# Kernel optimization log

Measured on AMD Instinct MI355X. Metric: run time of the kernel, lower is better.

The kernel has to match this reference:

```python
import jax, jax.numpy as jnp
import numpy as np

K = 8192
D = 512


def setup_inputs() -> dict:
    key = jax.random.key(0)
    k1, k2 = jax.random.split(key)
    x = jax.random.normal(k1, (32, 512, D), dtype=jnp.float32)
    # nn.Embedding weight init: uniform(-1/k, 1/k)
    codebook = jax.random.uniform(k2, (K, D), dtype=jnp.float32,
                                  minval=-1.0 / K, maxval=1.0 / K)
    return {"x": x, "codebook": codebook}


def reference(x, codebook):
    # flatten to [N, D]
    z_e = x.reshape(-1, x.shape[-1])
    # squared L2 distances: ||z||^2 - 2 z c^T + ||c||^2  -> [N, K]
    dists = (jnp.sum(z_e * z_e, axis=1, keepdims=True)
             - 2.0 * jnp.einsum('nd,kd->nk', z_e, codebook)
             + jnp.sum(codebook * codebook, axis=1)[None, :])
    indices = jnp.argmin(dists, axis=1)  # [N]
    z_q = codebook[indices]              # [N, D] gather
    # straight-through estimator: forward z_q, grad passes to z_e
    z_q_st = z_e + jax.lax.stop_gradient(z_q - z_e)
    # vq loss pulls codebook toward (detached) encoder outputs
    vq_loss = jnp.mean((z_q - jax.lax.stop_gradient(z_e)) ** 2)
    # commitment loss pulls encoder outputs toward (detached) codes
    commit_loss = jnp.mean((z_e - jax.lax.stop_gradient(z_q)) ** 2)
    z_q_out = z_q_st.reshape(x.shape)
    idx_out = indices.reshape(x.shape[:-1])
    return z_q_out, vq_loss, commit_loss, idx_out
```

## Files before the change

kernel.cpp:

```cpp
#include <hip/hip_runtime.h>

#define K_CODES 8192
#define D_DIM   512
#define N_ROWS  16384
#define NSPLIT  32
#define CAP     8
#define T2      2.0e-4f
#define LIST_CAP 32768

typedef __attribute__((ext_vector_type(8))) short bf16x8;
typedef __attribute__((ext_vector_type(4))) float f32x4;
typedef unsigned char uchar;
typedef unsigned short ushort;
typedef unsigned long long u64;

__device__ __forceinline__ unsigned fkey(float f) {
    unsigned b = __float_as_uint(f);
    return (b & 0x80000000u) ? ~b : (b | 0x80000000u);
}
__device__ __forceinline__ float finv(unsigned k) {
    return __uint_as_float((k & 0x80000000u) ? (k & 0x7fffffffu) : ~k);
}

__device__ __forceinline__ unsigned pk_bf16(float a, float b) {
    unsigned ua = __float_as_uint(a), ub = __float_as_uint(b);
    ua = (ua + 0x7fffu + ((ua >> 16) & 1u)) >> 16;
    ub = (ub + 0x7fffu + ((ub >> 16) & 1u)) & 0xffff0000u;
    return ua | ub;
}

__device__ __forceinline__ void gload_lds16(const void* g, void* l) {
    __builtin_amdgcn_global_load_lds(
        (const __attribute__((address_space(1))) unsigned int*)g,
        (__attribute__((address_space(3))) unsigned int*)l, 16, 0, 0);
}

__global__ void vq_prepass(const float* __restrict__ x, const float* __restrict__ cb,
                           unsigned* __restrict__ xb, unsigned* __restrict__ cbb,
                           float* __restrict__ sn, u64* __restrict__ keys,
                           int* __restrict__ count) {
    const int bid = blockIdx.x;
    const int t = threadIdx.x;
    if (bid < 6144) {
        const size_t gid = (size_t)bid * 256 + t;
        const size_t nx = (size_t)N_ROWS * D_DIM / 8;
        if (gid < nx) {
            const float4 f0 = ((const float4*)x)[gid * 2];
            const float4 f1 = ((const float4*)x)[gid * 2 + 1];
            ((uint4*)xb)[gid] = make_uint4(pk_bf16(f0.x, f0.y), pk_bf16(f0.z, f0.w),
                                           pk_bf16(f1.x, f1.y), pk_bf16(f1.z, f1.w));
        } else {
            const size_t g = gid - nx;
            const float4 f0 = ((const float4*)cb)[g * 2];
            const float4 f1 = ((const float4*)cb)[g * 2 + 1];
            ((uint4*)cbb)[g] = make_uint4(pk_bf16(f0.x, f0.y), pk_bf16(f0.z, f0.w),
                                          pk_bf16(f1.x, f1.y), pk_bf16(f1.z, f1.w));
        }
    } else {
        const int base = (bid - 6144) * 8;
        if (bid == 6144 && t == 0) *count = 0;
        if (t < 8) keys[base + t] = ~0ull;
        const int wave = t >> 6, lane = t & 63;
        const int row = base + wave * 2 + (lane >> 5);
        const int l = lane & 31, b = l >> 3, j = l & 7;
        const float* a = x + (size_t)row * D_DIM + b * 128 + j;
        float r = __fmul_rn(a[0], a[0]);
#pragma unroll
        for (int i = 1; i < 16; ++i) {
            const float v = a[i * 8];
            r = __fadd_rn(r, __fmul_rn(v, v));
        }
        r = __fadd_rn(r, __shfl_xor(r, 1));
        r = __fadd_rn(r, __shfl_xor(r, 2));
        r = __fadd_rn(r, __shfl_xor(r, 4));
        r = __fadd_rn(r, __shfl_xor(r, 8));
        r = __fadd_rn(r, __shfl_xor(r, 16));
        if (l == 0) sn[row] = r;
    }
}

__global__ __launch_bounds__(256)
void vq_sn(const float* __restrict__ x, float* __restrict__ sn,
           u64* __restrict__ keys, int* __restrict__ count) {
    const int t = threadIdx.x;
    const int base = blockIdx.x * 8;
    if (blockIdx.x == 0 && t == 0) *count = 0;
    if (t < 8) keys[base + t] = ~0ull;
    const int wave = t >> 6, lane = t & 63;
    const int row = base + wave * 2 + (lane >> 5);
    const int l = lane & 31, b = l >> 3, j = l & 7;
    const float* a = x + (size_t)row * D_DIM + b * 128 + j;
    float r = __fmul_rn(a[0], a[0]);
#pragma unroll
    for (int i = 1; i < 16; ++i) {
        const float v = a[i * 8];
        r = __fadd_rn(r, __fmul_rn(v, v));
    }
    r = __fadd_rn(r, __shfl_xor(r, 1));
    r = __fadd_rn(r, __shfl_xor(r, 2));
    r = __fadd_rn(r, __shfl_xor(r, 4));
    r = __fadd_rn(r, __shfl_xor(r, 8));
    r = __fadd_rn(r, __shfl_xor(r, 16));
    if (l == 0) sn[row] = r;
}

template<bool PRE>
__global__ __launch_bounds__(256, 2)
void vq_screen2(const float* __restrict__ x, const float* __restrict__ cb,
                const ushort* __restrict__ xb, const ushort* __restrict__ cbb,
                float* __restrict__ g_dmax, uchar* __restrict__ g_cnt,
                uchar* __restrict__ g_cand) {
    __shared__ ushort Ash[2][128 * 32];
    __shared__ ushort Bsh[2][256 * 32];
    __shared__ unsigned vkey[128];
    __shared__ int ccnt[128];
    __shared__ uchar clist[128][CAP];

    const int t    = threadIdx.x;
    const int w    = t >> 6, lane = t & 63;
    const int fr   = lane & 15;
    const int quad = lane >> 4;
    const int wr   = (w & 1) * 64;
    const int wc   = (w >> 1) * 128;
    const int row0  = blockIdx.y * 128;
    const int kbase = blockIdx.x * 256;

    if (t < 128) { vkey[t] = 0u; ccnt[t] = 0; }

    int aoff[4], boff[8];
#pragma unroll
    for (int i = 0; i < 4; ++i) {
        const int rw = wr + i * 16 + fr;
        aoff[i] = rw * 32 + ((quad ^ (rw >> 1)) & 3) * 8;
    }
#pragma unroll
    for (int j = 0; j < 8; ++j) {
        const int rw = wc + j * 16 + fr;
        boff[j] = rw * 32 + ((quad ^ (rw >> 1)) & 3) * 8;
    }

    f32x4 acc[4][8];
#pragma unroll
    for (int i = 0; i < 4; ++i)
#pragma unroll
        for (int j = 0; j < 8; ++j) acc[i][j] = (f32x4)0.0f;

    if (PRE) {
        const int la = lane >> 2;
        const int p  = lane & 3;
        const int ia0 = w * 2 + 0, rA0 = ia0 * 16 + la;
        const int ia1 = w * 2 + 1, rA1 = ia1 * 16 + la;
        const char* srcA0 = (const char*)xb + (size_t)(row0 + rA0) * 1024 + ((p ^ ((rA0 >> 1) & 3)) * 16);
        const char* srcA1 = (const char*)xb + (size_t)(row0 + rA1) * 1024 + ((p ^ ((rA1 >> 1) & 3)) * 16);
        const int dA0 = ia0 * 512, dA1 = ia1 * 512;
        const int ib0 = w * 4 + 0, rB0 = ib0 * 16 + la;
        const int ib1 = w * 4 + 1, rB1 = ib1 * 16 + la;
        const int ib2 = w * 4 + 2, rB2 = ib2 * 16 + la;
        const int ib3 = w * 4 + 3, rB3 = ib3 * 16 + la;
        const char* srcB0 = (const char*)cbb + (size_t)(kbase + rB0) * 1024 + ((p ^ ((rB0 >> 1) & 3)) * 16);
        const char* srcB1 = (const char*)cbb + (size_t)(kbase + rB1) * 1024 + ((p ^ ((rB1 >> 1) & 3)) * 16);
        const char* srcB2 = (const char*)cbb + (size_t)(kbase + rB2) * 1024 + ((p ^ ((rB2 >> 1) & 3)) * 16);
        const char* srcB3 = (const char*)cbb + (size_t)(kbase + rB3) * 1024 + ((p ^ ((rB3 >> 1) & 3)) * 16);

#define STAGE6(buf, slab) do {                                     \
        gload_lds16(srcA0 + (slab) * 64, &Ash[buf][dA0]);          \
        gload_lds16(srcA1 + (slab) * 64, &Ash[buf][dA1]);          \
        gload_lds16(srcB0 + (slab) * 64, &Bsh[buf][dB0]);          \
        gload_lds16(srcB1 + (slab) * 64, &Bsh[buf][dB1]);          \
        gload_lds16(srcB2 + (slab) * 64, &Bsh[buf][dB2]);          \
        gload_lds16(srcB3 + (slab) * 64, &Bsh[buf][dB3]);          \
    } while (0)
        const int dB0 = ib0 * 512, dB1 = ib1 * 512, dB2 = ib2 * 512, dB3 = ib3 * 512;

        STAGE6(0, 0);
        asm volatile("s_waitcnt vmcnt(0)" ::: "memory");
        __builtin_amdgcn_s_barrier();

#pragma unroll 2
        for (int dc = 0; dc < 16; ++dc) {
            const int cur = dc & 1;
            if (dc < 15) STAGE6(cur ^ 1, dc + 1);
            bf16x8 af[4], bfv[8];
#pragma unroll
            for (int i = 0; i < 4; ++i) af[i] = *(const bf16x8*)&Ash[cur][aoff[i]];
#pragma unroll
            for (int j = 0; j < 8; ++j) bfv[j] = *(const bf16x8*)&Bsh[cur][boff[j]];
#pragma unroll
            for (int i = 0; i < 4; ++i)
#pragma unroll
                for (int j = 0; j < 8; ++j)
                    acc[i][j] = __builtin_amdgcn_mfma_f32_16x16x32_bf16(af[i], bfv[j], acc[i][j], 0, 0, 0);
            asm volatile("s_waitcnt vmcnt(0)" ::: "memory");
            __builtin_amdgcn_s_barrier();
        }
#undef STAGE6
    } else {
        const int r = t >> 1, h = t & 1;
        const int sA = (r >> 1) & 3;
        const int ca0 = (2 * h) ^ sA;
        ushort* awp0 = &Ash[0][r * 32 + ca0 * 8];
        ushort* awp1 = &Ash[0][r * 32 + (ca0 ^ 1) * 8];
        const int sB = (t >> 1) & 3;
        ushort* bwp0 = &Bsh[0][t * 32 + (0 ^ sB) * 8];
        ushort* bwp1 = &Bsh[0][t * 32 + (1 ^ sB) * 8];
        ushort* bwp2 = &Bsh[0][t * 32 + (2 ^ sB) * 8];
        ushort* bwp3 = &Bsh[0][t * 32 + (3 ^ sB) * 8];
        const char* gA = (const char*)(x  + (size_t)(row0 + r) * D_DIM + h * 16);
        const char* gB = (const char*)(cb + (size_t)(kbase + t) * D_DIM);
        for (int dc = 0; dc < 16; ++dc) {
            const float4* fa = (const float4*)(gA + dc * 128);
            float4 f0 = fa[0], f1 = fa[1], f2 = fa[2], f3 = fa[3];
            uint4 a0 = make_uint4(pk_bf16(f0.x, f0.y), pk_bf16(f0.z, f0.w),
                                  pk_bf16(f1.x, f1.y), pk_bf16(f1.z, f1.w));
            uint4 a1 = make_uint4(pk_bf16(f2.x, f2.y), pk_bf16(f2.z, f2.w),
                                  pk_bf16(f3.x, f3.y), pk_bf16(f3.z, f3.w));
            const float4* fb = (const float4*)(gB + dc * 128);
            float4 g0 = fb[0], g1 = fb[1], g2 = fb[2], g3 = fb[3];
            float4 g4 = fb[4], g5 = fb[5], g6 = fb[6], g7 = fb[7];
            uint4 b0 = make_uint4(pk_bf16(g0.x, g0.y), pk_bf16(g0.z, g0.w),
                                  pk_bf16(g1.x, g1.y), pk_bf16(g1.z, g1.w));
            uint4 b1 = make_uint4(pk_bf16(g2.x, g2.y), pk_bf16(g2.z, g2.w),
                                  pk_bf16(g3.x, g3.y), pk_bf16(g3.z, g3.w));
            uint4 b2 = make_uint4(pk_bf16(g4.x, g4.y), pk_bf16(g4.z, g4.w),
                                  pk_bf16(g5.x, g5.y), pk_bf16(g5.z, g5.w));
            uint4 b3 = make_uint4(pk_bf16(g6.x, g6.y), pk_bf16(g6.z, g6.w),
                                  pk_bf16(g7.x, g7.y), pk_bf16(g7.z, g7.w));
            __syncthreads();
            *(uint4*)awp0 = a0; *(uint4*)awp1 = a1;
            *(uint4*)bwp0 = b0; *(uint4*)bwp1 = b1;
            *(uint4*)bwp2 = b2; *(uint4*)bwp3 = b3;
            __syncthreads();
            bf16x8 af[4], bfv[8];
#pragma unroll
            for (int i = 0; i < 4; ++i) af[i] = *(const bf16x8*)&Ash[0][aoff[i]];
#pragma unroll
            for (int j = 0; j < 8; ++j) bfv[j] = *(const bf16x8*)&Bsh[0][boff[j]];
#pragma unroll
            for (int i = 0; i < 4; ++i)
#pragma unroll
                for (int j = 0; j < 8; ++j)
                    acc[i][j] = __builtin_amdgcn_mfma_f32_16x16x32_bf16(af[i], bfv[j], acc[i][j], 0, 0, 0);
        }
    }

    __syncthreads();
#pragma unroll
    for (int i = 0; i < 4; ++i)
#pragma unroll
        for (int rg = 0; rg < 4; ++rg) {
            float m = acc[i][0][rg];
#pragma unroll
            for (int j = 1; j < 8; ++j) m = fmaxf(m, acc[i][j][rg]);
            m = fmaxf(m, __shfl_xor(m, 1));
            m = fmaxf(m, __shfl_xor(m, 2));
            m = fmaxf(m, __shfl_xor(m, 4));
            m = fmaxf(m, __shfl_xor(m, 8));
            if (fr == 0) atomicMax(&vkey[wr + i * 16 + quad * 4 + rg], fkey(m));
        }
    __syncthreads();
#pragma unroll
    for (int i = 0; i < 4; ++i)
#pragma unroll
        for (int rg = 0; rg < 4; ++rg) {
            const int row = wr + i * 16 + quad * 4 + rg;
            const float thr = finv(vkey[row]) - T2;
#pragma unroll
            for (int j = 0; j < 8; ++j) {
                if (acc[i][j][rg] >= thr) {
                    int p = atomicAdd(&ccnt[row], 1);
                    if (p < CAP) clist[row][p] = (uchar)(wc + j * 16 + fr);
                }
            }
        }
    __syncthreads();
    if (t < 128) {
        const size_t o = (size_t)(row0 + t) * NSPLIT + blockIdx.x;
        g_dmax[o] = finv(vkey[t]);
        int c = ccnt[t];
        g_cnt[o] = (uchar)(c > 255 ? 255 : c);
        ((uint2*)g_cand)[o] = *(const uint2*)clist[t];
    }
}

__global__ __launch_bounds__(256)
void vq_build(const float* __restrict__ g_dmax, const uchar* __restrict__ g_cnt,
              const uchar* __restrict__ g_cand, int2* __restrict__ list,
              int* __restrict__ count, float* __restrict__ idx_f) {
    const int row = blockIdx.x * blockDim.x + threadIdx.x;
    const int lane = threadIdx.x & 63;
    const float* dm = g_dmax + (size_t)row * NSPLIT;
    float g = dm[0];
#pragma unroll
    for (int s = 1; s < NSPLIT; ++s) g = fmaxf(g, dm[s]);
    const float thr = g - T2;

    int tot = 0, first = -1;
    for (int s = 0; s < NSPLIT; ++s) {
        if (dm[s] < thr) continue;
        const size_t o = (size_t)row * NSPLIT + s;
        const int c = g_cnt[o];
        tot += (c > CAP) ? 256 : c;
        if (first < 0) first = s * 256 + g_cand[o * CAP];
    }
    idx_f[row] = (float)first;

    const int need = (tot > 1) ? tot : 0;
    int scan = need;
#pragma unroll
    for (int d = 1; d < 64; d <<= 1) {
        const int v = __shfl_up(scan, d, 64);
        if (lane >= d) scan += v;
    }
    const int wtot = __shfl(scan, 63, 64);
    int base = 0;
    if (lane == 63 && wtot > 0) base = atomicAdd(count, wtot);
    base = __shfl(base, 63, 64);
    if (need == 0) return;
    int pos = base + scan - need;

    for (int s = 0; s < NSPLIT; ++s) {
        if (dm[s] < thr) continue;
        const size_t o = (size_t)row * NSPLIT + s;
        const int c = g_cnt[o];
        if (c > CAP) {
            for (int u = 0; u < 256; ++u, ++pos)
                if (pos < LIST_CAP) list[pos] = make_int2(row, s * 256 + u);
        } else {
            for (int u = 0; u < c; ++u, ++pos)
                if (pos < LIST_CAP) list[pos] = make_int2(row, s * 256 + g_cand[o * CAP + u]);
        }
    }
}

__device__ __forceinline__ float np_einsum_dot(const float* __restrict__ a,
                                               const float* __restrict__ b) {
    float S0 = 0.f, S1 = 0.f, S2 = 0.f, S3 = 0.f;
    for (int i = 0; i < D_DIM; i += 16) {
        S0 = __fadd_rn(S0, __fmul_rn(a[i + 12], b[i + 12]));
        S1 = __fadd_rn(S1, __fmul_rn(a[i + 13], b[i + 13]));
        S2 = __fadd_rn(S2, __fmul_rn(a[i + 14], b[i + 14]));
        S3 = __fadd_rn(S3, __fmul_rn(a[i + 15], b[i + 15]));
        S0 = __fadd_rn(S0, __fmul_rn(a[i +  8], b[i +  8]));
        S1 = __fadd_rn(S1, __fmul_rn(a[i +  9], b[i +  9]));
        S2 = __fadd_rn(S2, __fmul_rn(a[i + 10], b[i + 10]));
        S3 = __fadd_rn(S3, __fmul_rn(a[i + 11], b[i + 11]));
        S0 = __fadd_rn(S0, __fmul_rn(a[i +  4], b[i +  4]));
        S1 = __fadd_rn(S1, __fmul_rn(a[i +  5], b[i +  5]));
        S2 = __fadd_rn(S2, __fmul_rn(a[i +  6], b[i +  6]));
        S3 = __fadd_rn(S3, __fmul_rn(a[i +  7], b[i +  7]));
        S0 = __fadd_rn(S0, __fmul_rn(a[i +  0], b[i +  0]));
        S1 = __fadd_rn(S1, __fmul_rn(a[i +  1], b[i +  1]));
        S2 = __fadd_rn(S2, __fmul_rn(a[i +  2], b[i +  2]));
        S3 = __fadd_rn(S3, __fmul_rn(a[i +  3], b[i +  3]));
    }
    return __fadd_rn(__fadd_rn(S0, S1), __fadd_rn(S2, S3));
}

__global__ __launch_bounds__(256)
void vq_replay(const float* __restrict__ x, const float* __restrict__ cb,
               const float* __restrict__ sn, const int2* __restrict__ list,
               const int* __restrict__ count, u64* __restrict__ keys) {
    const int i = blockIdx.x * blockDim.x + threadIdx.x;
    int n = *count; if (n > LIST_CAP) n = LIST_CAP;
    if (i >= n) return;
    const int2 e = list[i];
    const float* zr = x + (size_t)e.x * D_DIM;
    const float d = __fadd_rn(sn[e.x],
                              __fmul_rn(-2.0f, np_einsum_dot(zr, cb + (size_t)e.y * D_DIM)));
    const u64 key = ((u64)fkey(d) << 32) | (unsigned)e.y;
    atomicMin(&keys[e.x], key);
}

__global__ void vq_gather_kernel(const float* __restrict__ x,
                                 const float* __restrict__ cb,
                                 const u64* __restrict__ keys,
                                 float* __restrict__ idx_f,
                                 float* __restrict__ zq_out,
                                 double* __restrict__ psum) {
    const int row = blockIdx.x;
    const int t   = threadIdx.x;
    const u64 ky = keys[row];
    const int k = (ky != ~0ull) ? (int)(ky & 0xffffffffu) : (int)idx_f[row];
    const float4 c  = ((const float4*)(cb + (size_t)k   * D_DIM))[t];
    const float4 xv = ((const float4*)(x  + (size_t)row * D_DIM))[t];
    float4 o;
    o.x = __fadd_rn(xv.x, __fsub_rn(c.x, xv.x));
    o.y = __fadd_rn(xv.y, __fsub_rn(c.y, xv.y));
    o.z = __fadd_rn(xv.z, __fsub_rn(c.z, xv.z));
    o.w = __fadd_rn(xv.w, __fsub_rn(c.w, xv.w));
    ((float4*)(zq_out + (size_t)row * D_DIM))[t] = o;
    const double d0 = (double)c.x - (double)xv.x;
    const double d1 = (double)c.y - (double)xv.y;
    const double d2 = (double)c.z - (double)xv.z;
    const double d3 = (double)c.w - (double)xv.w;
    double s = d0 * d0 + d1 * d1 + d2 * d2 + d3 * d3;
#pragma unroll
    for (int off = 32; off > 0; off >>= 1) s += __shfl_xor(s, off, 64);
    __shared__ double red[2];
    if ((t & 63) == 0) red[t >> 6] = s;
    __syncthreads();
    if (t == 0) {
        psum[row] = red[0] + red[1];
        idx_f[row] = (float)k;
    }
}

__global__ void vq_finalize2(const double* __restrict__ psum,
                             float* __restrict__ losses) {
    __shared__ double red[4];
    const int t = threadIdx.x;
    double s = 0.0;
    for (int i = t; i < N_ROWS; i += 256) s += psum[i];
#pragma unroll
    for (int off = 32; off > 0; off >>= 1) s += __shfl_xor(s, off, 64);
    if ((t & 63) == 0) red[t >> 6] = s;
    __syncthreads();
    if (t == 0) {
        const double tot = red[0] + red[1] + red[2] + red[3];
        const float l = (float)(tot / (double)((size_t)N_ROWS * D_DIM));
        losses[0] = l;
        losses[1] = l;
    }
}

extern "C" void kernel_launch(void* const* d_in, const int* in_sizes, int n_in,
                              void* d_out, int out_size, void* d_ws, size_t ws_size,
                              hipStream_t stream) {
    const float* x  = (const float*)d_in[0];
    const float* cb = (const float*)d_in[1];
    float* out    = (float*)d_out;
    float* zq     = out;
    float* losses = out + (size_t)N_ROWS * D_DIM;
    float* idx_f  = losses + 2;
    char* ws = (char*)d_ws;

    const bool pre = (ws_size >= ((size_t)32 << 20));
    char* base = pre ? (ws + ((size_t)24 << 20)) : ws;

    float*  g_dmax = (float*)(base);
    uchar*  g_cnt  = (uchar*)(base + (2048u << 10));
    uchar*  g_cand = (uchar*)(base + (2560u << 10));
    float*  sn     = (float*)(base + (6656u << 10));
    u64*    keys   = (u64*)  (base + (6720u << 10));
    int2*   list   = (int2*) (base + (6848u << 10));
    int*    count  = (int*)  (base + (7104u << 10));
    double* psum   = (double*)(base + (7168u << 10));

    if (pre) {
        ushort* xb  = (ushort*)ws;
        ushort* cbb = (ushort*)(ws + ((size_t)16 << 20));
        hipLaunchKernelGGL(vq_prepass, dim3(8192), dim3(256), 0, stream,
                           x, cb, (unsigned*)xb, (unsigned*)cbb, sn, keys, count);
        hipLaunchKernelGGL((vq_screen2<true>), dim3(K_CODES / 256, N_ROWS / 128), dim3(256), 0, stream,
                           x, cb, xb, cbb, g_dmax, g_cnt, g_cand);
    } else {
        hipLaunchKernelGGL(vq_sn, dim3(N_ROWS / 8), dim3(256), 0, stream,
                           x, sn, keys, count);
        hipLaunchKernelGGL((vq_screen2<false>), dim3(K_CODES / 256, N_ROWS / 128), dim3(256), 0, stream,
                           x, cb, (const ushort*)nullptr, (const ushort*)nullptr,
                           g_dmax, g_cnt, g_cand);
    }
    hipLaunchKernelGGL(vq_build, dim3(N_ROWS / 256), dim3(256), 0, stream,
                       g_dmax, g_cnt, g_cand, list, count, idx_f);
    hipLaunchKernelGGL(vq_replay, dim3(LIST_CAP / 256), dim3(256), 0, stream,
                       x, cb, sn, list, count, keys);
    hipLaunchKernelGGL(vq_gather_kernel, dim3(N_ROWS), dim3(128), 0, stream,
                       x, cb, keys, idx_f, zq, psum);
    hipLaunchKernelGGL(vq_finalize2, dim3(1), dim3(256), 0, stream,
                       psum, losses);
}
```

Baseline: 394.7 us.

## Deepen LDS prefetch pipeline and remap block IDs for codebook L2 locality

The bf16 screening GEMM now keeps two slabs in flight: it waits with vmcnt(6) instead of draining all loads each iteration, so global-to-LDS copies overlap the MFMA compute. It also adds a barrier before each buffer is reloaded. Block indices are permuted so that consecutively scheduled blocks share codebook tiles and spread across row tiles, which is meant to improve L2 reuse. The output slot uses the remapped split index. The extra barrier per iteration adds some sync cost.

Result: no change. 389.4 us (-1.3%).

```diff
diff --git a/kernel.cpp b/kernel.cpp
--- a/kernel.cpp
+++ b/kernel.cpp
@@ -122,8 +122,13 @@
     const int quad = lane >> 4;
     const int wr   = (w & 1) * 64;
     const int wc   = (w >> 1) * 128;
-    const int row0  = blockIdx.y * 128;
-    const int kbase = blockIdx.x * 256;
+
+    const int lin = blockIdx.x + 32 * blockIdx.y;
+    const int nl  = ((lin & 7) << 9) | (lin >> 3);
+    const int kb  = nl & 31;
+    const int rb  = nl >> 5;
+    const int row0  = rb * 128;
+    const int kbase = kb * 256;
 
     if (t < 128) { vkey[t] = 0u; ccnt[t] = 0; }
 
@@ -144,6 +149,19 @@
     for (int i = 0; i < 4; ++i)
 #pragma unroll
         for (int j = 0; j < 8; ++j) acc[i][j] = (f32x4)0.0f;
+
+#define COMPUTE(buf) do {                                                          \
+        bf16x8 af[4], bfv[8];                                                      \
+        _Pragma("unroll")                                                          \
+        for (int i_ = 0; i_ < 4; ++i_) af[i_] = *(const bf16x8*)&Ash[buf][aoff[i_]]; \
+        _Pragma("unroll")                                                          \
+        for (int j_ = 0; j_ < 8; ++j_) bfv[j_] = *(const bf16x8*)&Bsh[buf][boff[j_]]; \
+        _Pragma("unroll")                                                          \
+        for (int i_ = 0; i_ < 4; ++i_)                                             \
+        _Pragma("unroll")                                                          \
+            for (int j_ = 0; j_ < 8; ++j_)                                         \
+                acc[i_][j_] = __builtin_amdgcn_mfma_f32_16x16x32_bf16(af[i_], bfv[j_], acc[i_][j_], 0, 0, 0); \
+    } while (0)
 
     if (PRE) {
         const int la = lane >> 2;
@@ -161,6 +179,7 @@
         const char* srcB1 = (const char*)cbb + (size_t)(kbase + rB1) * 1024 + ((p ^ ((rB1 >> 1) & 3)) * 16);
         const char* srcB2 = (const char*)cbb + (size_t)(kbase + rB2) * 1024 + ((p ^ ((rB2 >> 1) & 3)) * 16);
         const char* srcB3 = (const char*)cbb + (size_t)(kbase + rB3) * 1024 + ((p ^ ((rB3 >> 1) & 3)) * 16);
+        const int dB0 = ib0 * 512, dB1 = ib1 * 512, dB2 = ib2 * 512, dB3 = ib3 * 512;
 
 #define STAGE6(buf, slab) do {                                     \
         gload_lds16(srcA0 + (slab) * 64, &Ash[buf][dA0]);          \
@@ -170,29 +189,25 @@
         gload_lds16(srcB2 + (slab) * 64, &Bsh[buf][dB2]);          \
         gload_lds16(srcB3 + (slab) * 64, &Bsh[buf][dB3]);          \
     } while (0)
-        const int dB0 = ib0 * 512, dB1 = ib1 * 512, dB2 = ib2 * 512, dB3 = ib3 * 512;
 
         STAGE6(0, 0);
+        STAGE6(1, 1);
+
+#pragma unroll 2
+        for (int dc = 0; dc < 14; ++dc) {
+            const int cur = dc & 1;
+            asm volatile("s_waitcnt vmcnt(6)" ::: "memory");
+            __builtin_amdgcn_s_barrier();
+            COMPUTE(cur);
+            __builtin_amdgcn_s_barrier();
+            STAGE6(cur, dc + 2);
+        }
+        asm volatile("s_waitcnt vmcnt(6)" ::: "memory");
+        __builtin_amdgcn_s_barrier();
+        COMPUTE(0);
         asm volatile("s_waitcnt vmcnt(0)" ::: "memory");
         __builtin_amdgcn_s_barrier();
-
-#pragma unroll 2
-        for (int dc = 0; dc < 16; ++dc) {
-            const int cur = dc & 1;
-            if (dc < 15) STAGE6(cur ^ 1, dc + 1);
-            bf16x8 af[4], bfv[8];
-#pragma unroll
-            for (int i = 0; i < 4; ++i) af[i] = *(const bf16x8*)&Ash[cur][aoff[i]];
-#pragma unroll
-            for (int j = 0; j < 8; ++j) bfv[j] = *(const bf16x8*)&Bsh[cur][boff[j]];
-#pragma unroll
-            for (int i = 0; i < 4; ++i)
-#pragma unroll
-                for (int j = 0; j < 8; ++j)
-                    acc[i][j] = __builtin_amdgcn_mfma_f32_16x16x32_bf16(af[i], bfv[j], acc[i][j], 0, 0, 0);
-            asm volatile("s_waitcnt vmcnt(0)" ::: "memory");
-            __builtin_amdgcn_s_barrier();
-        }
+        COMPUTE(1);
 #undef STAGE6
     } else {
         const int r = t >> 1, h = t & 1;
@@ -230,18 +245,10 @@
             *(uint4*)bwp0 = b0; *(uint4*)bwp1 = b1;
             *(uint4*)bwp2 = b2; *(uint4*)bwp3 = b3;
             __syncthreads();
-            bf16x8 af[4], bfv[8];
-#pragma unroll
-            for (int i = 0; i < 4; ++i) af[i] = *(const bf16x8*)&Ash[0][aoff[i]];
-#pragma unroll
-            for (int j = 0; j < 8; ++j) bfv[j] = *(const bf16x8*)&Bsh[0][boff[j]];
-#pragma unroll
-            for (int i = 0; i < 4; ++i)
-#pragma unroll
-                for (int j = 0; j < 8; ++j)
-                    acc[i][j] = __builtin_amdgcn_mfma_f32_16x16x32_bf16(af[i], bfv[j], acc[i][j], 0, 0, 0);
-        }
-    }
+            COMPUTE(0);
+        }
+    }
+#undef COMPUTE
 
     __syncthreads();
 #pragma unroll
@@ -274,7 +281,7 @@
         }
     __syncthreads();
     if (t < 128) {
-        const size_t o = (size_t)(row0 + t) * NSPLIT + blockIdx.x;
+        const size_t o = (size_t)(row0 + t) * NSPLIT + kb;
         g_dmax[o] = finv(vkey[t]);
         int c = ccnt[t];
         g_cnt[o] = (uchar)(c > 255 ? 255 : c);
```

## Triple-buffer screen GEMM with split-phase loads and swap grid order

Applied to the files above, without the earlier changes.

Converts the bf16 MFMA screening loop from a double buffer to a triple buffer with prefetch two slabs ahead. Each slab's loads and MFMAs are split into two halves interleaved with barriers and scheduling priority hints. The grid dimensions are swapped so neighbouring blocks share a codebook slice, which improves L2 reuse. This raises LDS use per block and adds extra barriers per iteration, which may limit occupancy or add sync cost.

Measured after the change: 388.9 us. Within noise of the previous version (-1.5%).

```diff
diff --git a/kernel.cpp b/kernel.cpp
--- a/kernel.cpp
+++ b/kernel.cpp
@@ -110,8 +110,8 @@
                 const ushort* __restrict__ xb, const ushort* __restrict__ cbb,
                 float* __restrict__ g_dmax, uchar* __restrict__ g_cnt,
                 uchar* __restrict__ g_cand) {
-    __shared__ ushort Ash[2][128 * 32];
-    __shared__ ushort Bsh[2][256 * 32];
+    __shared__ ushort Ash[3][128 * 32];
+    __shared__ ushort Bsh[3][256 * 32];
     __shared__ unsigned vkey[128];
     __shared__ int ccnt[128];
     __shared__ uchar clist[128][CAP];
@@ -122,8 +122,9 @@
     const int quad = lane >> 4;
     const int wr   = (w & 1) * 64;
     const int wc   = (w >> 1) * 128;
-    const int row0  = blockIdx.y * 128;
-    const int kbase = blockIdx.x * 256;
+    const int ks    = blockIdx.y;
+    const int row0  = blockIdx.x * 128;
+    const int kbase = ks * 256;
 
     if (t < 128) { vkey[t] = 0u; ccnt[t] = 0; }
 
@@ -161,6 +162,7 @@
         const char* srcB1 = (const char*)cbb + (size_t)(kbase + rB1) * 1024 + ((p ^ ((rB1 >> 1) & 3)) * 16);
         const char* srcB2 = (const char*)cbb + (size_t)(kbase + rB2) * 1024 + ((p ^ ((rB2 >> 1) & 3)) * 16);
         const char* srcB3 = (const char*)cbb + (size_t)(kbase + rB3) * 1024 + ((p ^ ((rB3 >> 1) & 3)) * 16);
+        const int dB0 = ib0 * 512, dB1 = ib1 * 512, dB2 = ib2 * 512, dB3 = ib3 * 512;
 
 #define STAGE6(buf, slab) do {                                     \
         gload_lds16(srcA0 + (slab) * 64, &Ash[buf][dA0]);          \
@@ -170,29 +172,64 @@
         gload_lds16(srcB2 + (slab) * 64, &Bsh[buf][dB2]);          \
         gload_lds16(srcB3 + (slab) * 64, &Bsh[buf][dB3]);          \
     } while (0)
-        const int dB0 = ib0 * 512, dB1 = ib1 * 512, dB2 = ib2 * 512, dB3 = ib3 * 512;
+#define SBAR0() __builtin_amdgcn_sched_barrier(0)
 
         STAGE6(0, 0);
-        asm volatile("s_waitcnt vmcnt(0)" ::: "memory");
-        __builtin_amdgcn_s_barrier();
-
-#pragma unroll 2
+        STAGE6(1, 1);
+        SBAR0();
+
+#pragma unroll
         for (int dc = 0; dc < 16; ++dc) {
-            const int cur = dc & 1;
-            if (dc < 15) STAGE6(cur ^ 1, dc + 1);
+            const int cur = dc % 3;
+            const int nxt = (dc + 2) % 3;
+            if (dc < 15) { asm volatile("s_waitcnt vmcnt(6)" ::: "memory"); }
+            else         { asm volatile("s_waitcnt vmcnt(0)" ::: "memory"); }
+            SBAR0();
+            __builtin_amdgcn_s_barrier();
+            SBAR0();
             bf16x8 af[4], bfv[8];
 #pragma unroll
             for (int i = 0; i < 4; ++i) af[i] = *(const bf16x8*)&Ash[cur][aoff[i]];
 #pragma unroll
-            for (int j = 0; j < 8; ++j) bfv[j] = *(const bf16x8*)&Bsh[cur][boff[j]];
+            for (int j = 0; j < 4; ++j) bfv[j] = *(const bf16x8*)&Bsh[cur][boff[j]];
+            if (dc <= 13) {
+                gload_lds16(srcA0 + (dc + 2) * 64, &Ash[nxt][dA0]);
+                gload_lds16(srcA1 + (dc + 2) * 64, &Ash[nxt][dA1]);
+                gload_lds16(srcB0 + (dc + 2) * 64, &Bsh[nxt][dB0]);
+            }
+            SBAR0();
+            __builtin_amdgcn_s_barrier();
+            asm volatile("s_waitcnt lgkmcnt(0)" ::: "memory");
+            SBAR0();
+            __builtin_amdgcn_s_setprio(1);
 #pragma unroll
             for (int i = 0; i < 4; ++i)
 #pragma unroll
-                for (int j = 0; j < 8; ++j)
+                for (int j = 0; j < 4; ++j)
                     acc[i][j] = __builtin_amdgcn_mfma_f32_16x16x32_bf16(af[i], bfv[j], acc[i][j], 0, 0, 0);
-            asm volatile("s_waitcnt vmcnt(0)" ::: "memory");
+            __builtin_amdgcn_s_setprio(0);
+            SBAR0();
+#pragma unroll
+            for (int j = 4; j < 8; ++j) bfv[j] = *(const bf16x8*)&Bsh[cur][boff[j]];
+            if (dc <= 13) {
+                gload_lds16(srcB1 + (dc + 2) * 64, &Bsh[nxt][dB1]);
+                gload_lds16(srcB2 + (dc + 2) * 64, &Bsh[nxt][dB2]);
+                gload_lds16(srcB3 + (dc + 2) * 64, &Bsh[nxt][dB3]);
+            }
+            SBAR0();
             __builtin_amdgcn_s_barrier();
-        }
+            asm volatile("s_waitcnt lgkmcnt(0)" ::: "memory");
+            SBAR0();
+            __builtin_amdgcn_s_setprio(1);
+#pragma unroll
+            for (int i = 0; i < 4; ++i)
+#pragma unroll
+                for (int j = 4; j < 8; ++j)
+                    acc[i][j] = __builtin_amdgcn_mfma_f32_16x16x32_bf16(af[i], bfv[j], acc[i][j], 0, 0, 0);
+            __builtin_amdgcn_s_setprio(0);
+            SBAR0();
+        }
+#undef SBAR0
 #undef STAGE6
     } else {
         const int r = t >> 1, h = t & 1;
@@ -274,7 +311,7 @@
         }
     __syncthreads();
     if (t < 128) {
-        const size_t o = (size_t)(row0 + t) * NSPLIT + blockIdx.x;
+        const size_t o = (size_t)(row0 + t) * NSPLIT + ks;
         g_dmax[o] = finv(vkey[t]);
         int c = ccnt[t];
         g_cnt[o] = (uchar)(c > 255 ? 255 : c);
@@ -451,12 +488,12 @@
         ushort* cbb = (ushort*)(ws + ((size_t)16 << 20));
         hipLaunchKernelGGL(vq_prepass, dim3(8192), dim3(256), 0, stream,
                            x, cb, (unsigned*)xb, (unsigned*)cbb, sn, keys, count);
-        hipLaunchKernelGGL((vq_screen2<true>), dim3(K_CODES / 256, N_ROWS / 128), dim3(256), 0, stream,
+        hipLaunchKernelGGL((vq_screen2<true>), dim3(N_ROWS / 128, K_CODES / 256), dim3(256), 0, stream,
                            x, cb, xb, cbb, g_dmax, g_cnt, g_cand);
     } else {
         hipLaunchKernelGGL(vq_sn, dim3(N_ROWS / 8), dim3(256), 0, stream,
                            x, sn, keys, count);
-        hipLaunchKernelGGL((vq_screen2<false>), dim3(K_CODES / 256, N_ROWS / 128), dim3(256), 0, stream,
+        hipLaunchKernelGGL((vq_screen2<false>), dim3(N_ROWS / 128, K_CODES / 256), dim3(256), 0, stream,
                            x, cb, (const ushort*)nullptr, (const ushort*)nullptr,
                            g_dmax, g_cnt, g_cand);
     }
```
